# Optimization experiments

Measured on AMD Instinct MI355X. Metric: run time of the kernel, lower is better.

Reference implementation:

```python
import jax, jax.numpy as jnp
import numpy as np
import math

B, S, D, H = 2, 2048, 512, 8  # batch, seq, d_hidden (= per-head dim here), n_heads


def _rope(x):
    # x: [B, H, S, D]; standard interleaved RoPE with base 10000
    b, h, s, d = x.shape
    inv_freq = 1.0 / (10000.0 ** (jnp.arange(0, d, 2, dtype=jnp.float32) / d))  # [d/2]
    ang = jnp.arange(s, dtype=jnp.float32)[:, None] * inv_freq[None, :]          # [S, d/2]
    cos, sin = jnp.cos(ang), jnp.sin(ang)
    x1, x2 = x[..., 0::2], x[..., 1::2]
    r1 = x1 * cos - x2 * sin
    r2 = x1 * sin + x2 * cos
    return jnp.stack([r1, r2], axis=-1).reshape(b, h, s, d).astype(x.dtype)


def setup_inputs() -> dict:
    key = jax.random.key(0)
    kq, k1, k2, k3, k4 = jax.random.split(key, 5)
    std = 0.02
    return {
        "q": jax.random.normal(kq, (B, S, D), dtype=jnp.float32),
        "W_q": jax.random.normal(k1, (H, D, D), dtype=jnp.float32) * std,
        "W_k": jax.random.normal(k2, (H, D, D), dtype=jnp.float32) * std,
        "W_v": jax.random.normal(k3, (H, D, D), dtype=jnp.float32) * std,
        "W_o": jax.random.normal(k4, (H * D, D), dtype=jnp.float32) * std,
    }


def reference(q, W_q, W_k, W_v, W_o):
    b, s, d = q.shape
    h = W_q.shape[0]
    scale = 1.0 / math.sqrt(d)
    qh = jnp.einsum('bsz,hzd->bhsd', q, W_q)
    kh = jnp.einsum('bsz,hzd->bhsd', q, W_k)
    vh = jnp.einsum('bsz,hzd->bhsd', q, W_v)
    qh = _rope(qh)
    kh = _rope(kh)
    scores = jnp.einsum('bhqd,bhkd->bhqk', qh, kh) * scale
    causal = jnp.triu(jnp.ones((s, s), dtype=bool), k=1)  # True above diagonal
    scores = jnp.where(causal, -jnp.inf, scores)
    probs = jax.nn.softmax(scores, axis=-1)  # dropout is identity in eval
    # NOTE: faithful to the original (transposed) einsum: contracts over the
    # query index z of probs with the sequence index z of v.
    out = jnp.einsum('bhzs,bhzd->bhsd', probs, vh)
    out = out.transpose(0, 2, 1, 3).reshape(b, s, h * d)
    return jnp.einsum('bsz,zd->bsd', out, W_o)
```

## Files before the change

### kernel.cpp

```cpp
#include <hip/hip_runtime.h>
#include <hip/hip_bf16.h>
#include <math.h>
#include <stdint.h>

#define BB 2
#define SS 2048
#define DD 512
#define HH 8
#define NTOK (BB*SS)
#define NQKV (3*HH*DD)
#define BHD  (HH*DD)
#define NBH  (BB*HH)
#define NTILE 136

typedef __attribute__((ext_vector_type(8))) short short8v;
typedef __attribute__((ext_vector_type(4))) float floatx4;

__device__ __forceinline__ unsigned short f2bf(float f) {
  unsigned int u = __builtin_bit_cast(unsigned int, f);
  u = (u + 0x7FFFu + ((u >> 16) & 1u)) >> 16;
  return (unsigned short)u;
}
__device__ __forceinline__ float bf2f(unsigned short s) {
  unsigned int u = ((unsigned int)s) << 16;
  return __builtin_bit_cast(float, u);
}
__device__ __forceinline__ void async16(const void* g, void* l) {
  __builtin_amdgcn_global_load_lds(
      (const __attribute__((address_space(1))) unsigned int*)g,
      (__attribute__((address_space(3))) unsigned int*)l, 16, 0, 0);
}
#define WAITVM(N) asm volatile("s_waitcnt vmcnt(" #N ")" ::: "memory")
#define BAR() __builtin_amdgcn_s_barrier()

__global__ void k_convert_q(const float* __restrict__ q, unsigned short* __restrict__ qbf) {
  int i = (blockIdx.x * 256 + threadIdx.x) * 4;
  const float4 v = *(const float4*)&q[i];
  ushort4 o;
  o.x = f2bf(v.x); o.y = f2bf(v.y); o.z = f2bf(v.z); o.w = f2bf(v.w);
  *(ushort4*)&qbf[i] = o;
}

__global__ void k_rope_tab(float* __restrict__ rope) {
  const int idx = blockIdx.x * 256 + threadIdx.x;
  const int s = idx >> 8, dp = idx & 255;
  const float inv = exp2f(-13.287712379549449f * (1.0f/256.0f) * (float)dp);
  float sn, cs;
  __sincosf((float)s * inv, &sn, &cs);
  rope[(size_t)idx * 2]     = cs;
  rope[(size_t)idx * 2 + 1] = sn;
}

__global__ void k_prep_w(const float* __restrict__ Wq, const float* __restrict__ Wk,
                         const float* __restrict__ Wv, const float* __restrict__ Wo,
                         unsigned short* __restrict__ Wcat, unsigned short* __restrict__ Wot) {
  __shared__ float t[32][33];
  const int z = blockIdx.z;
  const float* in; unsigned short* out; int inLD, outLD;
  float sc = 1.0f;
  if (z < 24) {
    int tsel = z / 8, h = z % 8;
    const float* w = (tsel == 0) ? Wq : (tsel == 1) ? Wk : Wv;
    if (tsel == 0) sc = 0.044194173824159216f;
    in = w + (size_t)h * DD * DD;
    out = Wcat + ((size_t)tsel * BHD + (size_t)h * DD) * DD;
    inLD = DD; outLD = DD;
  } else {
    int k = z - 24;
    in = Wo + (size_t)k * DD * DD;
    out = Wot + (size_t)k * DD;
    inLD = DD; outLD = BHD;
  }
  const int tx = threadIdx.x, ty = threadIdx.y;
  const int bx = blockIdx.x * 32, by = blockIdx.y * 32;
  for (int kk = 0; kk < 4; ++kk)
    t[ty + 8*kk][tx] = in[(size_t)(by + ty + 8*kk) * inLD + bx + tx];
  __syncthreads();
  for (int kk = 0; kk < 4; ++kk)
    out[(size_t)(bx + ty + 8*kk) * outLD + by + tx] = f2bf(t[tx][ty + 8*kk] * sc);
}

__global__ __launch_bounds__(256, 2)
void k_qkv(const unsigned short* __restrict__ Abf, const unsigned short* __restrict__ Bt,
           const float* __restrict__ ropeT,
           unsigned short* __restrict__ Qr, unsigned short* __restrict__ Kr,
           unsigned short* __restrict__ Vt) {
  __shared__ short As[2][128*32];
  __shared__ short Bs[2][256*32];
  const int tid = threadIdx.x;
  const int lin = blockIdx.y * 32 + blockIdx.x;
  const int lin2 = (lin & 7) * 192 + (lin >> 3);
  const int m0 = (lin2 & 31) * 128;
  const int n0 = (lin2 >> 5) * 256;
  const int wave = tid >> 6, lane = tid & 63, qd = lane >> 4, c = lane & 15;
  const int wm = (wave >> 1) * 64, wn = (wave & 1) * 128;
  floatx4 acc[4][8] = {};
  const int e0 = tid * 8;
  const int r0 = e0 >> 5, c0 = e0 & 31;
  auto STAGE = [&](int buf, int k0) {
    async16(&Abf[(size_t)(m0 + r0      ) * 512 + k0 + c0], &As[buf][e0]);
    async16(&Abf[(size_t)(m0 + r0 +  64) * 512 + k0 + c0], &As[buf][e0 + 2048]);
    async16(&Bt [(size_t)(n0 + r0      ) * 512 + k0 + c0], &Bs[buf][e0]);
    async16(&Bt [(size_t)(n0 + r0 +  64) * 512 + k0 + c0], &Bs[buf][e0 + 2048]);
    async16(&Bt [(size_t)(n0 + r0 + 128) * 512 + k0 + c0], &Bs[buf][e0 + 4096]);
    async16(&Bt [(size_t)(n0 + r0 + 192) * 512 + k0 + c0], &Bs[buf][e0 + 6144]);
  };
  STAGE(0, 0);
  for (int k0 = 0; k0 < 512; k0 += 32) {
    const int cur = (k0 >> 5) & 1;
    if (k0 < 480) { STAGE(cur ^ 1, k0 + 32); WAITVM(6); }
    else          { WAITVM(0); }
    BAR();
    short8v a[4], bfr[8];
    for (int mt = 0; mt < 4; ++mt) a[mt]   = *(const short8v*)&As[cur][(wm + mt*16 + c)*32 + qd*8];
    for (int nt = 0; nt < 8; ++nt) bfr[nt] = *(const short8v*)&Bs[cur][(wn + nt*16 + c)*32 + qd*8];
    for (int mt = 0; mt < 4; ++mt)
      for (int nt = 0; nt < 8; ++nt)
        acc[mt][nt] = __builtin_amdgcn_mfma_f32_16x16x32_bf16(a[mt], bfr[nt], acc[mt][nt], 0, 0, 0);
    BAR();
  }
  const int tsel = n0 >> 12;
  const int h = (n0 >> 9) & 7;
  const int bat = m0 >> 11;
  const int bh = bat * HH + h;
  const int dloc = (n0 & 511) + wn;
  if (tsel < 2) {
    unsigned short* dst = (tsel == 0) ? Qr : Kr;
    const int dp0 = (dloc >> 1) + (c >> 1);
    const unsigned int sgn = (c & 1) ? 0u : 0x80000000u;
    for (int mt = 0; mt < 4; ++mt) {
      const int mrow = (m0 & 2047) + wm + mt*16 + qd*4;
      for (int r = 0; r < 4; ++r) {
        const int s = mrow + r;
        const float2* rp = (const float2*)&ropeT[((size_t)s * 256 + dp0) * 2];
        const size_t ob = ((size_t)bh * SS + s) * DD;
        for (int nt = 0; nt < 8; ++nt) {
          const float2 tt = rp[nt * 8];
          const float v = acc[mt][nt][r];
          float p = __shfl_xor(v, 1, 64);
          p = __builtin_bit_cast(float, __builtin_bit_cast(unsigned int, p) ^ sgn);
          dst[ob + dloc + nt*16 + c] = f2bf(fmaf(p, tt.y, v * tt.x));
        }
      }
    }
  } else {
    for (int nt = 0; nt < 8; ++nt) {
      const int d = dloc + nt*16 + c;
      const size_t vbase = ((size_t)bh * DD + d) * SS;
      for (int mt = 0; mt < 4; ++mt) {
        const int s = (m0 & 2047) + wm + mt*16 + qd*4;
        ushort4 u;
        u.x = f2bf(acc[mt][nt][0]); u.y = f2bf(acc[mt][nt][1]);
        u.z = f2bf(acc[mt][nt][2]); u.w = f2bf(acc[mt][nt][3]);
        *(ushort4*)&Vt[vbase + s] = u;
      }
    }
  }
}

__global__ __launch_bounds__(256)
void k_scores(const unsigned short* __restrict__ Qr, const unsigned short* __restrict__ Kr,
              unsigned short* __restrict__ Eg, float* __restrict__ lsum) {
  __shared__ short UN[17408];
  unsigned short* ET = (unsigned short*)UN;
  const int tid = threadIdx.x;
  const int lin = blockIdx.y * 136 + blockIdx.x;
  const int lin2 = (lin & 7) * 272 + (lin >> 3);
  const int bh = lin2 / 136;
  const int t = lin2 % 136;
  int zb = 0;
  while (((zb + 1) * (zb + 2)) / 2 <= t) ++zb;
  const int st = t - (zb * (zb + 1)) / 2;
  const int z0 = zb * 128, s0 = st * 128;
  const int wave = tid >> 6, lane = tid & 63, qd = lane >> 4, c = lane & 15;
  const int wm = (wave >> 1) * 64, wn = (wave & 1) * 64;
  const size_t qb = (size_t)bh * SS * DD;
  floatx4 acc[4][4] = {};
  const int e0 = tid * 8, e1 = e0 + 2048;
  const int r0 = e0 >> 5, c0 = e0 & 31, r1 = e1 >> 5, c1 = e1 & 31;
  auto STAGE = [&](int buf, int k0) {
    short* A = UN + buf * 4096;
    short* B = UN + 8192 + buf * 4096;
    async16(&Qr[qb + (size_t)(z0 + r0) * 512 + k0 + c0], &A[e0]);
    async16(&Qr[qb + (size_t)(z0 + r1) * 512 + k0 + c1], &A[e1]);
    async16(&Kr[qb + (size_t)(s0 + r0) * 512 + k0 + c0], &B[e0]);
    async16(&Kr[qb + (size_t)(s0 + r1) * 512 + k0 + c1], &B[e1]);
  };
  STAGE(0, 0);
  for (int kk = 0; kk < 16; ++kk) {
    const int cur = kk & 1;
    if (kk < 15) { STAGE(cur ^ 1, (kk + 1) * 32); WAITVM(4); }
    else         { WAITVM(0); }
    BAR();
    const short* Asp = UN + cur * 4096;
    const short* Bsp = UN + 8192 + cur * 4096;
    short8v a[4], bfr[4];
    for (int mt = 0; mt < 4; ++mt) a[mt]   = *(const short8v*)&Asp[(wm + mt*16 + c)*32 + qd*8];
    for (int nt = 0; nt < 4; ++nt) bfr[nt] = *(const short8v*)&Bsp[(wn + nt*16 + c)*32 + qd*8];
    for (int mt = 0; mt < 4; ++mt)
      for (int nt = 0; nt < 4; ++nt)
        acc[mt][nt] = __builtin_amdgcn_mfma_f32_16x16x32_bf16(a[mt], bfr[nt], acc[mt][nt], 0, 0, 0);
    BAR();
  }
  const bool diag = (st == zb);
  for (int mt = 0; mt < 4; ++mt) {
    const int zl = wm + mt*16 + qd*4;
    float rs[4] = {0.f, 0.f, 0.f, 0.f};
    for (int nt = 0; nt < 4; ++nt) {
      const int sl = wn + nt*16 + c;
      for (int r = 0; r < 4; ++r) {
        float ev = __expf(acc[mt][nt][r]);
        if (diag && (sl > zl + r)) ev = 0.f;
        acc[mt][nt][r] = ev;
        rs[r] += ev;
      }
    }
    for (int off = 1; off < 16; off <<= 1)
      for (int r = 0; r < 4; ++r) rs[r] += __shfl_xor(rs[r], off, 64);
    if (c == 0)
      for (int r = 0; r < 4; ++r)
        atomicAdd(&lsum[(size_t)bh * SS + z0 + zl + r], rs[r]);
  }
  for (int mt = 0; mt < 4; ++mt) {
    const int zl = wm + mt*16 + qd*4;
    for (int nt = 0; nt < 4; ++nt) {
      const int sl = wn + nt*16 + c;
      ushort4 u;
      u.x = f2bf(acc[mt][nt][0]); u.y = f2bf(acc[mt][nt][1]);
      u.z = f2bf(acc[mt][nt][2]); u.w = f2bf(acc[mt][nt][3]);
      *(ushort4*)&ET[sl * 136 + zl] = u;
    }
  }
  __syncthreads();
  const size_t tb = ((size_t)bh * NTILE + t) * 16384;
  for (int it = 0; it < 8; ++it) {
    const int e = it * 2048 + tid * 8;
    const int row = e >> 7, col = e & 127;
    *(short8v*)&Eg[tb + row * 128 + col] = *(const short8v*)&ET[row * 136 + col];
  }
}

__global__ void k_vscale(unsigned short* __restrict__ Vt, const float* __restrict__ lsum) {
  const int idx = (blockIdx.x * 256 + threadIdx.x) * 8;
  const int z = idx & (SS - 1);
  const int bh = idx >> 20;
  short8v v = *(const short8v*)&Vt[idx];
  const float* lp = &lsum[(size_t)bh * SS + z];
  short8v o;
  for (int i = 0; i < 8; ++i)
    o[i] = (short)f2bf(bf2f((unsigned short)v[i]) / lp[i]);
  *(short8v*)&Vt[idx] = o;
}

__global__ __launch_bounds__(256)
void k_pv(const unsigned short* __restrict__ Eg, const unsigned short* __restrict__ Vs,
          unsigned short* __restrict__ Ocat) {
  __shared__ short Vl[2][2][128*32];
  __shared__ short El[2][2][128*32];
  const int tid = threadIdx.x;
  const int lin = (blockIdx.z * 8 + blockIdx.y) * 4 + blockIdx.x;
  const int lin2 = (lin & 7) * 64 + (lin >> 3);
  const int d0 = (lin2 & 3) * 128;
  const int pr = (lin2 >> 2) & 7;
  const int bh = lin2 >> 5;
  const int bat = bh >> 3, h = bh & 7;
  const int wave = tid >> 6, lane = tid & 63, qd = lane >> 4, c = lane & 15;
  const int wm = (wave >> 1) * 64, wn = (wave & 1) * 64;
  const size_t vbb = (size_t)bh * DD * SS;
  const int e = tid * 8;
  auto STAGE = [&](int buf, int zb, int half, int st) {
    const size_t tb = ((size_t)bh * NTILE + (zb * (zb + 1)) / 2 + st) * 16384;
    const int zbase = zb * 128 + half * 64;
    for (int i = 0; i < 4; ++i) {
      const int ee = e + i * 2048;
      const int kc = ee >> 12, row = (ee >> 5) & 127, col = ee & 31;
      async16(&Vs[vbb + (size_t)(d0 + row) * SS + zbase + kc * 32 + col], &Vl[buf][kc][row * 32 + col]);
    }
    for (int i = 0; i < 4; ++i) {
      const int ee = e + i * 2048;
      const int kc = ee >> 12, row = (ee >> 5) & 127, col = ee & 31;
      async16(&Eg[tb + (size_t)row * 128 + half * 64 + kc * 32 + col], &El[buf][kc][row * 32 + col]);
    }
  };
  for (int sel = 0; sel < 2; ++sel) {
    const int st = sel ? (15 - pr) : pr;
    const int s0 = st * 128;
    floatx4 acc[4][4] = {};
    const int nst = (16 - st) * 2;
    STAGE(0, st, 0, st);
    for (int q2 = 0; q2 < nst; ++q2) {
      const int cur = q2 & 1;
      if (q2 + 1 < nst) { STAGE(cur ^ 1, st + ((q2 + 1) >> 1), (q2 + 1) & 1, st); WAITVM(8); }
      else              { WAITVM(0); }
      BAR();
      for (int kc = 0; kc < 2; ++kc) {
        short8v a[4], b[4];
        for (int dt = 0; dt < 4; ++dt) a[dt] = *(const short8v*)&Vl[cur][kc][(wm + dt*16 + c)*32 + qd*8];
        for (int nt = 0; nt < 4; ++nt) b[nt] = *(const short8v*)&El[cur][kc][(wn + nt*16 + c)*32 + qd*8];
        for (int dt = 0; dt < 4; ++dt)
          for (int nt = 0; nt < 4; ++nt)
            acc[dt][nt] = __builtin_amdgcn_mfma_f32_16x16x32_bf16(a[dt], b[nt], acc[dt][nt], 0, 0, 0);
      }
      BAR();
    }
    for (int nt = 0; nt < 4; ++nt) {
      const int sg = s0 + wn + nt*16 + c;
      const size_t ob = ((size_t)(bat * SS + sg)) * BHD + (size_t)h * DD + d0;
      for (int dt = 0; dt < 4; ++dt) {
        const int dloc = wm + dt*16 + qd*4;
        ushort4 u;
        u.x = f2bf(acc[dt][nt][0]); u.y = f2bf(acc[dt][nt][1]);
        u.z = f2bf(acc[dt][nt][2]); u.w = f2bf(acc[dt][nt][3]);
        *(ushort4*)&Ocat[ob + dloc] = u;
      }
    }
  }
}

__global__ __launch_bounds__(256)
void k_oproj(const unsigned short* __restrict__ Ocat, const unsigned short* __restrict__ Wot,
             float* __restrict__ out) {
  __shared__ short As[2][2][128*32];
  __shared__ short Bs[2][2][128*32];
  const int tid = threadIdx.x;
  const int lin = (blockIdx.z * 4 + blockIdx.y) * 32 + blockIdx.x;
  const int lin2 = (lin & 7) * 64 + (lin >> 3);
  const int m0 = (lin2 & 31) * 128;
  const int rest = lin2 >> 5;
  const int n0 = (rest & 3) * 128;
  const int ks = (rest >> 2) * 1024;
  const int wave = tid >> 6, lane = tid & 63, qd = lane >> 4, c = lane & 15;
  const int wm = (wave >> 1) * 64, wn = (wave & 1) * 64;
  floatx4 acc[4][4] = {};
  const int e0 = tid * 8, e1 = e0 + 2048;
  const int r0 = e0 >> 5, c0 = e0 & 31, r1 = e1 >> 5, c1 = e1 & 31;
  auto STAGE = [&](int buf, int k0) {
    for (int kc = 0; kc < 2; ++kc) {
      const int kk = k0 + kc * 32;
      async16(&Ocat[(size_t)(m0 + r0) * BHD + kk + c0], &As[buf][kc][e0]);
      async16(&Ocat[(size_t)(m0 + r1) * BHD + kk + c1], &As[buf][kc][e1]);
      async16(&Wot [(size_t)(n0 + r0) * BHD + kk + c0], &Bs[buf][kc][e0]);
      async16(&Wot [(size_t)(n0 + r1) * BHD + kk + c1], &Bs[buf][kc][e1]);
    }
  };
  STAGE(0, ks);
  for (int t = 0; t < 16; ++t) {
    const int cur = t & 1;
    if (t < 15) { STAGE(cur ^ 1, ks + (t + 1) * 64); WAITVM(8); }
    else        { WAITVM(0); }
    BAR();
    for (int kc = 0; kc < 2; ++kc) {
      short8v a[4], b[4];
      for (int mt = 0; mt < 4; ++mt) a[mt] = *(const short8v*)&As[cur][kc][(wm + mt*16 + c)*32 + qd*8];
      for (int nt = 0; nt < 4; ++nt) b[nt] = *(const short8v*)&Bs[cur][kc][(wn + nt*16 + c)*32 + qd*8];
      for (int mt = 0; mt < 4; ++mt)
        for (int nt = 0; nt < 4; ++nt)
          acc[mt][nt] = __builtin_amdgcn_mfma_f32_16x16x32_bf16(a[mt], b[nt], acc[mt][nt], 0, 0, 0);
    }
    BAR();
  }
  for (int mt = 0; mt < 4; ++mt) {
    const int m = m0 + wm + mt*16 + qd*4;
    for (int nt = 0; nt < 4; ++nt) {
      const int n = n0 + wn + nt*16 + c;
      for (int r = 0; r < 4; ++r)
        atomicAdd(&out[(size_t)(m + r) * DD + n], acc[mt][nt][r]);
    }
  }
}

extern "C" void kernel_launch(void* const* d_in, const int* in_sizes, int n_in,
                              void* d_out, int out_size, void* d_ws, size_t ws_size,
                              hipStream_t stream) {
  const float* q  = (const float*)d_in[0];
  const float* Wq = (const float*)d_in[1];
  const float* Wk = (const float*)d_in[2];
  const float* Wv = (const float*)d_in[3];
  const float* Wo = (const float*)d_in[4];

  char* base = (char*)d_ws;
  unsigned short* Eg   = (unsigned short*)base;
  unsigned short* qbf  = (unsigned short*)base;
  unsigned short* Wcat = (unsigned short*)(base + 4194304);
  float*          rope = (float*)(base + 16777216);
  char* p = base + 71303168;
  unsigned short* Wot  = (unsigned short*)p; p += 4194304;
  unsigned short* Qr   = (unsigned short*)p;
  unsigned short* Ocat = (unsigned short*)p; p += 33554432;
  unsigned short* Kr   = (unsigned short*)p; p += 33554432;
  unsigned short* Vt   = (unsigned short*)p; p += 33554432;
  float*          lsum = (float*)p;

  hipMemsetAsync(lsum, 0, (size_t)NBH * SS * 4, stream);
  hipMemsetAsync(d_out, 0, (size_t)NTOK * DD * 4, stream);

  k_convert_q<<<NTOK*DD/1024, 256, 0, stream>>>(q, qbf);
  k_rope_tab<<<SS*256/256, 256, 0, stream>>>(rope);
  k_prep_w<<<dim3(16,16,32), dim3(32,8), 0, stream>>>(Wq, Wk, Wv, Wo, Wcat, Wot);
  k_qkv<<<dim3(32,48), 256, 0, stream>>>(qbf, Wcat, rope, Qr, Kr, Vt);
  k_scores<<<dim3(NTILE,16), 256, 0, stream>>>(Qr, Kr, Eg, lsum);
  k_vscale<<<NBH*DD*SS/(256*8), 256, 0, stream>>>(Vt, lsum);
  k_pv<<<dim3(4,8,16), 256, 0, stream>>>(Eg, Vt, Ocat);
  k_oproj<<<dim3(32,4,4), 256, 0, stream>>>(Ocat, Wot, (float*)d_out);
}
```

Baseline: 373.7 us.

## Switch GEMM kernels from double to triple-buffered async LDS pipelines

```diff
diff --git a/kernel.cpp b/kernel.cpp
--- a/kernel.cpp
+++ b/kernel.cpp
@@ -85,8 +85,8 @@
            const float* __restrict__ ropeT,
            unsigned short* __restrict__ Qr, unsigned short* __restrict__ Kr,
            unsigned short* __restrict__ Vt) {
-  __shared__ short As[2][128*32];
-  __shared__ short Bs[2][256*32];
+  __shared__ short As[3][128*32];
+  __shared__ short Bs[3][256*32];
   const int tid = threadIdx.x;
   const int lin = blockIdx.y * 32 + blockIdx.x;
   const int lin2 = (lin & 7) * 192 + (lin >> 3);
@@ -106,10 +106,13 @@
     async16(&Bt [(size_t)(n0 + r0 + 192) * 512 + k0 + c0], &Bs[buf][e0 + 6144]);
   };
   STAGE(0, 0);
-  for (int k0 = 0; k0 < 512; k0 += 32) {
-    const int cur = (k0 >> 5) & 1;
-    if (k0 < 480) { STAGE(cur ^ 1, k0 + 32); WAITVM(6); }
-    else          { WAITVM(0); }
+  STAGE(1, 32);
+#pragma unroll
+  for (int i = 0; i < 16; ++i) {
+    const int cur = i % 3;
+    if (i < 14)      { STAGE((i + 2) % 3, (i + 2) * 32); WAITVM(12); }
+    else if (i == 14){ WAITVM(6); }
+    else             { WAITVM(0); }
     BAR();
     short8v a[4], bfr[8];
     for (int mt = 0; mt < 4; ++mt) a[mt]   = *(const short8v*)&As[cur][(wm + mt*16 + c)*32 + qd*8];
@@ -161,7 +164,7 @@
 __global__ __launch_bounds__(256)
 void k_scores(const unsigned short* __restrict__ Qr, const unsigned short* __restrict__ Kr,
               unsigned short* __restrict__ Eg, float* __restrict__ lsum) {
-  __shared__ short UN[17408];
+  __shared__ short UN[24576];
   unsigned short* ET = (unsigned short*)UN;
   const int tid = threadIdx.x;
   const int lin = blockIdx.y * 136 + blockIdx.x;
@@ -180,20 +183,23 @@
   const int r0 = e0 >> 5, c0 = e0 & 31, r1 = e1 >> 5, c1 = e1 & 31;
   auto STAGE = [&](int buf, int k0) {
     short* A = UN + buf * 4096;
-    short* B = UN + 8192 + buf * 4096;
+    short* B = UN + 12288 + buf * 4096;
     async16(&Qr[qb + (size_t)(z0 + r0) * 512 + k0 + c0], &A[e0]);
     async16(&Qr[qb + (size_t)(z0 + r1) * 512 + k0 + c1], &A[e1]);
     async16(&Kr[qb + (size_t)(s0 + r0) * 512 + k0 + c0], &B[e0]);
     async16(&Kr[qb + (size_t)(s0 + r1) * 512 + k0 + c1], &B[e1]);
   };
   STAGE(0, 0);
+  STAGE(1, 32);
+#pragma unroll
   for (int kk = 0; kk < 16; ++kk) {
-    const int cur = kk & 1;
-    if (kk < 15) { STAGE(cur ^ 1, (kk + 1) * 32); WAITVM(4); }
-    else         { WAITVM(0); }
+    const int cur = kk % 3;
+    if (kk < 14)      { STAGE((kk + 2) % 3, (kk + 2) * 32); WAITVM(8); }
+    else if (kk == 14){ WAITVM(4); }
+    else              { WAITVM(0); }
     BAR();
     const short* Asp = UN + cur * 4096;
-    const short* Bsp = UN + 8192 + cur * 4096;
+    const short* Bsp = UN + 12288 + cur * 4096;
     short8v a[4], bfr[4];
     for (int mt = 0; mt < 4; ++mt) a[mt]   = *(const short8v*)&Asp[(wm + mt*16 + c)*32 + qd*8];
     for (int nt = 0; nt < 4; ++nt) bfr[nt] = *(const short8v*)&Bsp[(wn + nt*16 + c)*32 + qd*8];
@@ -255,8 +261,8 @@
 __global__ __launch_bounds__(256)
 void k_pv(const unsigned short* __restrict__ Eg, const unsigned short* __restrict__ Vs,
           unsigned short* __restrict__ Ocat) {
-  __shared__ short Vl[2][2][128*32];
-  __shared__ short El[2][2][128*32];
+  __shared__ short Vl[3][128*32];
+  __shared__ short El[3][128*32];
   const int tid = threadIdx.x;
   const int lin = (blockIdx.z * 8 + blockIdx.y) * 4 + blockIdx.x;
   const int lin2 = (lin & 7) * 64 + (lin >> 3);
@@ -268,40 +274,39 @@
   const int wm = (wave >> 1) * 64, wn = (wave & 1) * 64;
   const size_t vbb = (size_t)bh * DD * SS;
   const int e = tid * 8;
-  auto STAGE = [&](int buf, int zb, int half, int st) {
+  auto STAGE = [&](int buf, int zq, int st) {
+    const int zb = st + (zq >> 2);
     const size_t tb = ((size_t)bh * NTILE + (zb * (zb + 1)) / 2 + st) * 16384;
-    const int zbase = zb * 128 + half * 64;
-    for (int i = 0; i < 4; ++i) {
+    const int zin = (zq & 3) * 32;
+    const int zbase = zb * 128 + zin;
+    for (int i = 0; i < 2; ++i) {
       const int ee = e + i * 2048;
-      const int kc = ee >> 12, row = (ee >> 5) & 127, col = ee & 31;
-      async16(&Vs[vbb + (size_t)(d0 + row) * SS + zbase + kc * 32 + col], &Vl[buf][kc][row * 32 + col]);
-    }
-    for (int i = 0; i < 4; ++i) {
-      const int ee = e + i * 2048;
-      const int kc = ee >> 12, row = (ee >> 5) & 127, col = ee & 31;
-      async16(&Eg[tb + (size_t)row * 128 + half * 64 + kc * 32 + col], &El[buf][kc][row * 32 + col]);
+      const int row = ee >> 5, col = ee & 31;
+      async16(&Vs[vbb + (size_t)(d0 + row) * SS + zbase + col], &Vl[buf][row * 32 + col]);
+      async16(&Eg[tb + (size_t)row * 128 + zin + col], &El[buf][row * 32 + col]);
     }
   };
   for (int sel = 0; sel < 2; ++sel) {
     const int st = sel ? (15 - pr) : pr;
     const int s0 = st * 128;
     floatx4 acc[4][4] = {};
-    const int nst = (16 - st) * 2;
-    STAGE(0, st, 0, st);
+    const int nst = (16 - st) * 4;
+    STAGE(0, 0, st);
+    STAGE(1, 1, st);
+    int cur = 0;
     for (int q2 = 0; q2 < nst; ++q2) {
-      const int cur = q2 & 1;
-      if (q2 + 1 < nst) { STAGE(cur ^ 1, st + ((q2 + 1) >> 1), (q2 + 1) & 1, st); WAITVM(8); }
-      else              { WAITVM(0); }
+      if (q2 + 2 < nst)       { STAGE(cur ? cur - 1 : 2, q2 + 2, st); WAITVM(8); }
+      else if (q2 + 2 == nst) { WAITVM(4); }
+      else                    { WAITVM(0); }
       BAR();
-      for (int kc = 0; kc < 2; ++kc) {
-        short8v a[4], b[4];
-        for (int dt = 0; dt < 4; ++dt) a[dt] = *(const short8v*)&Vl[cur][kc][(wm + dt*16 + c)*32 + qd*8];
-        for (int nt = 0; nt < 4; ++nt) b[nt] = *(const short8v*)&El[cur][kc][(wn + nt*16 + c)*32 + qd*8];
-        for (int dt = 0; dt < 4; ++dt)
-          for (int nt = 0; nt < 4; ++nt)
-            acc[dt][nt] = __builtin_amdgcn_mfma_f32_16x16x32_bf16(a[dt], b[nt], acc[dt][nt], 0, 0, 0);
-      }
+      short8v a[4], b[4];
+      for (int dt = 0; dt < 4; ++dt) a[dt] = *(const short8v*)&Vl[cur][(wm + dt*16 + c)*32 + qd*8];
+      for (int nt = 0; nt < 4; ++nt) b[nt] = *(const short8v*)&El[cur][(wn + nt*16 + c)*32 + qd*8];
+      for (int dt = 0; dt < 4; ++dt)
+        for (int nt = 0; nt < 4; ++nt)
+          acc[dt][nt] = __builtin_amdgcn_mfma_f32_16x16x32_bf16(a[dt], b[nt], acc[dt][nt], 0, 0, 0);
       BAR();
+      cur = (cur == 2) ? 0 : cur + 1;
     }
     for (int nt = 0; nt < 4; ++nt) {
       const int sg = s0 + wn + nt*16 + c;
@@ -320,8 +325,8 @@
 __global__ __launch_bounds__(256)
 void k_oproj(const unsigned short* __restrict__ Ocat, const unsigned short* __restrict__ Wot,
              float* __restrict__ out) {
-  __shared__ short As[2][2][128*32];
-  __shared__ short Bs[2][2][128*32];
+  __shared__ short As[3][128*32];
+  __shared__ short Bs[3][128*32];
   const int tid = threadIdx.x;
   const int lin = (blockIdx.z * 4 + blockIdx.y) * 32 + blockIdx.x;
   const int lin2 = (lin & 7) * 64 + (lin >> 3);
@@ -335,29 +340,27 @@
   const int e0 = tid * 8, e1 = e0 + 2048;
   const int r0 = e0 >> 5, c0 = e0 & 31, r1 = e1 >> 5, c1 = e1 & 31;
   auto STAGE = [&](int buf, int k0) {
-    for (int kc = 0; kc < 2; ++kc) {
-      const int kk = k0 + kc * 32;
-      async16(&Ocat[(size_t)(m0 + r0) * BHD + kk + c0], &As[buf][kc][e0]);
-      async16(&Ocat[(size_t)(m0 + r1) * BHD + kk + c1], &As[buf][kc][e1]);
-      async16(&Wot [(size_t)(n0 + r0) * BHD + kk + c0], &Bs[buf][kc][e0]);
-      async16(&Wot [(size_t)(n0 + r1) * BHD + kk + c1], &Bs[buf][kc][e1]);
-    }
+    async16(&Ocat[(size_t)(m0 + r0) * BHD + k0 + c0], &As[buf][e0]);
+    async16(&Ocat[(size_t)(m0 + r1) * BHD + k0 + c1], &As[buf][e1]);
+    async16(&Wot [(size_t)(n0 + r0) * BHD + k0 + c0], &Bs[buf][e0]);
+    async16(&Wot [(size_t)(n0 + r1) * BHD + k0 + c1], &Bs[buf][e1]);
   };
   STAGE(0, ks);
-  for (int t = 0; t < 16; ++t) {
-    const int cur = t & 1;
-    if (t < 15) { STAGE(cur ^ 1, ks + (t + 1) * 64); WAITVM(8); }
-    else        { WAITVM(0); }
-    BAR();
-    for (int kc = 0; kc < 2; ++kc) {
-      short8v a[4], b[4];
-      for (int mt = 0; mt < 4; ++mt) a[mt] = *(const short8v*)&As[cur][kc][(wm + mt*16 + c)*32 + qd*8];
-      for (int nt = 0; nt < 4; ++nt) b[nt] = *(const short8v*)&Bs[cur][kc][(wn + nt*16 + c)*32 + qd*8];
-      for (int mt = 0; mt < 4; ++mt)
-        for (int nt = 0; nt < 4; ++nt)
-          acc[mt][nt] = __builtin_amdgcn_mfma_f32_16x16x32_bf16(a[mt], b[nt], acc[mt][nt], 0, 0, 0);
-    }
-    BAR();
+  STAGE(1, ks + 32);
+  int cur = 0;
+  for (int i = 0; i < 32; ++i) {
+    if (i < 30)      { STAGE(cur ? cur - 1 : 2, ks + (i + 2) * 32); WAITVM(8); }
+    else if (i == 30){ WAITVM(4); }
+    else             { WAITVM(0); }
+    BAR();
+    short8v a[4], b[4];
+    for (int mt = 0; mt < 4; ++mt) a[mt] = *(const short8v*)&As[cur][(wm + mt*16 + c)*32 + qd*8];
+    for (int nt = 0; nt < 4; ++nt) b[nt] = *(const short8v*)&Bs[cur][(wn + nt*16 + c)*32 + qd*8];
+    for (int mt = 0; mt < 4; ++mt)
+      for (int nt = 0; nt < 4; ++nt)
+        acc[mt][nt] = __builtin_amdgcn_mfma_f32_16x16x32_bf16(a[mt], b[nt], acc[mt][nt], 0, 0, 0);
+    BAR();
+    cur = (cur == 2) ? 0 : cur + 1;
   }
   for (int mt = 0; mt < 4; ++mt) {
     const int m = m0 + wm + mt*16 + qd*4;
```

Measured after the change: 376.6 us. About the same (+0.8%).

## Restructure QKV GEMM into 256x256 tiles with phased LDS pipeline

Applied to the files above, without the earlier changes.

```diff
diff --git a/kernel.cpp b/kernel.cpp
--- a/kernel.cpp
+++ b/kernel.cpp
@@ -80,78 +80,114 @@
     out[(size_t)(bx + ty + 8*kk) * outLD + by + tx] = f2bf(t[tx][ty + 8*kk] * sc);
 }
 
-__global__ __launch_bounds__(256, 2)
+__global__ __launch_bounds__(512, 1)
 void k_qkv(const unsigned short* __restrict__ Abf, const unsigned short* __restrict__ Bt,
            const float* __restrict__ ropeT,
            unsigned short* __restrict__ Qr, unsigned short* __restrict__ Kr,
            unsigned short* __restrict__ Vt) {
-  __shared__ short As[2][128*32];
-  __shared__ short Bs[2][256*32];
+  __shared__ short A_lds[2][2][128*64];
+  __shared__ short B_lds[2][2][128*64];
   const int tid = threadIdx.x;
-  const int lin = blockIdx.y * 32 + blockIdx.x;
-  const int lin2 = (lin & 7) * 192 + (lin >> 3);
-  const int m0 = (lin2 & 31) * 128;
-  const int n0 = (lin2 >> 5) * 256;
+  const int lin2 = (blockIdx.x & 7) * 96 + (blockIdx.x >> 3);
+  const int m0 = (lin2 & 15) * 256;
+  const int n0 = (lin2 >> 4) * 256;
   const int wave = tid >> 6, lane = tid & 63, qd = lane >> 4, c = lane & 15;
-  const int wm = (wave >> 1) * 64, wn = (wave & 1) * 128;
-  floatx4 acc[4][8] = {};
-  const int e0 = tid * 8;
-  const int r0 = e0 >> 5, c0 = e0 & 31;
-  auto STAGE = [&](int buf, int k0) {
-    async16(&Abf[(size_t)(m0 + r0      ) * 512 + k0 + c0], &As[buf][e0]);
-    async16(&Abf[(size_t)(m0 + r0 +  64) * 512 + k0 + c0], &As[buf][e0 + 2048]);
-    async16(&Bt [(size_t)(n0 + r0      ) * 512 + k0 + c0], &Bs[buf][e0]);
-    async16(&Bt [(size_t)(n0 + r0 +  64) * 512 + k0 + c0], &Bs[buf][e0 + 2048]);
-    async16(&Bt [(size_t)(n0 + r0 + 128) * 512 + k0 + c0], &Bs[buf][e0 + 4096]);
-    async16(&Bt [(size_t)(n0 + r0 + 192) * 512 + k0 + c0], &Bs[buf][e0 + 6144]);
-  };
-  STAGE(0, 0);
-  for (int k0 = 0; k0 < 512; k0 += 32) {
-    const int cur = (k0 >> 5) & 1;
-    if (k0 < 480) { STAGE(cur ^ 1, k0 + 32); WAITVM(6); }
-    else          { WAITVM(0); }
-    BAR();
-    short8v a[4], bfr[8];
-    for (int mt = 0; mt < 4; ++mt) a[mt]   = *(const short8v*)&As[cur][(wm + mt*16 + c)*32 + qd*8];
-    for (int nt = 0; nt < 8; ++nt) bfr[nt] = *(const short8v*)&Bs[cur][(wn + nt*16 + c)*32 + qd*8];
-    for (int mt = 0; mt < 4; ++mt)
-      for (int nt = 0; nt < 8; ++nt)
-        acc[mt][nt] = __builtin_amdgcn_mfma_f32_16x16x32_bf16(a[mt], bfr[nt], acc[mt][nt], 0, 0, 0);
-    BAR();
-  }
+  const int wm = (wave >> 2) * 128;
+  const int wn = (wave & 3) * 64;
+  const int Ha = wm >> 7;
+  const int Hb = wn >> 7;
+  const int brw = (wn & 64) + c;
+  const int cw = c & 7;
+  const int s0q = (qd ^ cw) * 8;
+  const int s1q = ((4 | qd) ^ cw) * 8;
+  const int trow = tid >> 3;
+  const int scol = ((tid & 7) ^ (trow & 7)) * 8;
+  const int tlin = tid * 8;
+  floatx4 acc[8][4] = {};
+  short8v ar[4][2], br0[2][2], br1[2][2];
+
+#define STG_A(T, H) if ((T) < 8) { \
+    async16(&Abf[(size_t)(m0 + (H)*128 + trow     ) * 512 + (T)*64 + scol], &A_lds[(T)&1][H][tlin]); \
+    async16(&Abf[(size_t)(m0 + (H)*128 + trow + 64) * 512 + (T)*64 + scol], &A_lds[(T)&1][H][tlin + 4096]); }
+#define STG_B(T, H) if ((T) < 8) { \
+    async16(&Bt [(size_t)(n0 + (H)*128 + trow     ) * 512 + (T)*64 + scol], &B_lds[(T)&1][H][tlin]); \
+    async16(&Bt [(size_t)(n0 + (H)*128 + trow + 64) * 512 + (T)*64 + scol], &B_lds[(T)&1][H][tlin + 4096]); }
+
+#define PH(DB, MH, NH, BR, DOA, DOB, STAGE, WAITC) { \
+    if (DOA) { \
+      _Pragma("unroll") for (int mf = 0; mf < 4; ++mf) { \
+        const int ra = ((MH)*64 + mf*16 + c) * 64; \
+        ar[mf][0] = *(const short8v*)&A_lds[DB][Ha][ra + s0q]; \
+        ar[mf][1] = *(const short8v*)&A_lds[DB][Ha][ra + s1q]; } } \
+    if (DOB) { \
+      _Pragma("unroll") for (int nf = 0; nf < 2; ++nf) { \
+        const int rb = (brw + (NH)*32 + nf*16) * 64; \
+        BR[nf][0] = *(const short8v*)&B_lds[DB][Hb][rb + s0q]; \
+        BR[nf][1] = *(const short8v*)&B_lds[DB][Hb][rb + s1q]; } } \
+    STAGE; \
+    BAR(); \
+    asm volatile("s_waitcnt lgkmcnt(0)" ::: "memory"); \
+    __builtin_amdgcn_s_setprio(1); \
+    _Pragma("unroll") for (int mf = 0; mf < 4; ++mf) \
+      _Pragma("unroll") for (int nf = 0; nf < 2; ++nf) { \
+        acc[(MH)*4+mf][(NH)*2+nf] = __builtin_amdgcn_mfma_f32_16x16x32_bf16(ar[mf][0], BR[nf][0], acc[(MH)*4+mf][(NH)*2+nf], 0, 0, 0); \
+        acc[(MH)*4+mf][(NH)*2+nf] = __builtin_amdgcn_mfma_f32_16x16x32_bf16(ar[mf][1], BR[nf][1], acc[(MH)*4+mf][(NH)*2+nf], 0, 0, 0); } \
+    __builtin_amdgcn_s_setprio(0); \
+    WAITC; \
+    BAR(); }
+
+  STG_A(0, 0); STG_A(0, 1); STG_B(0, 0); STG_B(0, 1); STG_A(1, 0);
+  WAITVM(2); BAR();
+
+  for (int it = 0; it < 4; ++it) {
+    const int t1 = 2*it + 1, t2 = 2*it + 2, t3 = 2*it + 3;
+    PH(0, 0, 0, br0, 1, 1, STG_A(t1, 1), ;)
+    PH(0, 0, 1, br1, 0, 1, STG_B(t1, 0), ;)
+    PH(0, 1, 0, br0, 1, 0, STG_B(t1, 1), ;)
+    PH(0, 1, 1, br1, 0, 0, STG_A(t2, 0), if (it < 3) { WAITVM(2); } else { WAITVM(0); })
+    PH(1, 0, 0, br0, 1, 1, STG_A(t2, 1), ;)
+    PH(1, 0, 1, br1, 0, 1, STG_B(t2, 0), ;)
+    PH(1, 1, 0, br0, 1, 0, STG_B(t2, 1), ;)
+    PH(1, 1, 1, br1, 0, 0, STG_A(t3, 0), if (it < 3) { WAITVM(2); })
+  }
+#undef PH
+#undef STG_A
+#undef STG_B
+
   const int tsel = n0 >> 12;
   const int h = (n0 >> 9) & 7;
   const int bat = m0 >> 11;
   const int bh = bat * HH + h;
-  const int dloc = (n0 & 511) + wn;
+  const int colw = (n0 & 511) + wn;
   if (tsel < 2) {
     unsigned short* dst = (tsel == 0) ? Qr : Kr;
-    const int dp0 = (dloc >> 1) + (c >> 1);
+    const int dp0 = (colw >> 1) + (c >> 1);
     const unsigned int sgn = (c & 1) ? 0u : 0x80000000u;
-    for (int mt = 0; mt < 4; ++mt) {
-      const int mrow = (m0 & 2047) + wm + mt*16 + qd*4;
+    for (int mi = 0; mi < 8; ++mi) {
+      const int mrow = (m0 & 2047) + wm + (mi >> 2)*64 + (mi & 3)*16 + qd*4;
       for (int r = 0; r < 4; ++r) {
         const int s = mrow + r;
         const float2* rp = (const float2*)&ropeT[((size_t)s * 256 + dp0) * 2];
         const size_t ob = ((size_t)bh * SS + s) * DD;
-        for (int nt = 0; nt < 8; ++nt) {
-          const float2 tt = rp[nt * 8];
-          const float v = acc[mt][nt][r];
+        for (int ni = 0; ni < 4; ++ni) {
+          const int dof = (ni >> 1)*32 + (ni & 1)*16;
+          const float2 tt = rp[dof >> 1];
+          const float v = acc[mi][ni][r];
           float p = __shfl_xor(v, 1, 64);
           p = __builtin_bit_cast(float, __builtin_bit_cast(unsigned int, p) ^ sgn);
-          dst[ob + dloc + nt*16 + c] = f2bf(fmaf(p, tt.y, v * tt.x));
+          dst[ob + colw + dof + c] = f2bf(fmaf(p, tt.y, v * tt.x));
         }
       }
     }
   } else {
-    for (int nt = 0; nt < 8; ++nt) {
-      const int d = dloc + nt*16 + c;
+    for (int ni = 0; ni < 4; ++ni) {
+      const int d = colw + (ni >> 1)*32 + (ni & 1)*16 + c;
       const size_t vbase = ((size_t)bh * DD + d) * SS;
-      for (int mt = 0; mt < 4; ++mt) {
-        const int s = (m0 & 2047) + wm + mt*16 + qd*4;
+      for (int mi = 0; mi < 8; ++mi) {
+        const int s = (m0 & 2047) + wm + (mi >> 2)*64 + (mi & 3)*16 + qd*4;
         ushort4 u;
-        u.x = f2bf(acc[mt][nt][0]); u.y = f2bf(acc[mt][nt][1]);
-        u.z = f2bf(acc[mt][nt][2]); u.w = f2bf(acc[mt][nt][3]);
+        u.x = f2bf(acc[mi][ni][0]); u.y = f2bf(acc[mi][ni][1]);
+        u.z = f2bf(acc[mi][ni][2]); u.w = f2bf(acc[mi][ni][3]);
         *(ushort4*)&Vt[vbase + s] = u;
       }
     }
@@ -397,7 +433,7 @@
   k_convert_q<<<NTOK*DD/1024, 256, 0, stream>>>(q, qbf);
   k_rope_tab<<<SS*256/256, 256, 0, stream>>>(rope);
   k_prep_w<<<dim3(16,16,32), dim3(32,8), 0, stream>>>(Wq, Wk, Wv, Wo, Wcat, Wot);
-  k_qkv<<<dim3(32,48), 256, 0, stream>>>(qbf, Wcat, rope, Qr, Kr, Vt);
+  k_qkv<<<768, 512, 0, stream>>>(qbf, Wcat, rope, Qr, Kr, Vt);
   k_scores<<<dim3(NTILE,16), 256, 0, stream>>>(Qr, Kr, Eg, lsum);
   k_vscale<<<NBH*DD*SS/(256*8), 256, 0, stream>>>(Vt, lsum);
   k_pv<<<dim3(4,8,16), 256, 0, stream>>>(Eg, Vt, Ocat);
```

New measurement: 367.0 us, median of 3. About the same (-1.8%).
